# Kernel optimization log

Measured on AMD Instinct MI355X. Metric: run time of the kernel, lower is better.

The kernel has to match this reference:

```python
import jax, jax.numpy as jnp
import numpy as np

C_IN = 256
C_OUT = 256
NUM_HEADS = 4
C_HEAD = C_OUT // NUM_HEADS  # 64
ALPHA = 0.2
NEG_FILL = -9e15


def setup_inputs() -> dict:
    key = jax.random.key(0)
    k1, k2, k3, k4, k5 = jax.random.split(key, 5)
    B, N = 1, 4096
    node_feats = jax.random.normal(k1, (B, N, C_IN), dtype=jnp.float32)
    adj_matrix = jax.random.randint(k2, (B, N, N), 0, 2, dtype=jnp.int32)
    # xavier_uniform with gain=1.414 on projection weight (fan_in=C_IN, fan_out=C_OUT)
    lim_w = 1.414 * np.sqrt(6.0 / (C_IN + C_OUT))
    W = jax.random.uniform(k3, (C_IN, C_OUT), dtype=jnp.float32, minval=-lim_w, maxval=lim_w)
    b = jnp.zeros((C_OUT,), dtype=jnp.float32)
    lim_a = 1.414 * np.sqrt(6.0 / (NUM_HEADS + 2 * C_HEAD))
    a = jax.random.uniform(k4, (NUM_HEADS, 2 * C_HEAD), dtype=jnp.float32, minval=-lim_a, maxval=lim_a)
    return {"node_feats": node_feats, "adj_matrix": adj_matrix, "W": W, "b": b, "a": a}


def reference(node_feats, adj_matrix, W, b, a):
    B, N, _ = node_feats.shape
    # linear projection -> (B, N, H, C_HEAD)
    feats = (node_feats @ W + b).reshape(B, N, NUM_HEADS, C_HEAD)
    # attention logit for edge (i -> j): a_src . h_i + a_dst . h_j, per head
    a_src, a_dst = a[:, :C_HEAD], a[:, C_HEAD:]
    src = jnp.einsum('bnhc,hc->bnh', feats, a_src)  # indexed by row i
    dst = jnp.einsum('bnhc,hc->bnh', feats, a_dst)  # indexed by col j
    logits = src[:, :, None, :] + dst[:, None, :, :]  # (B, N, N, H)
    logits = jnp.where(logits >= 0, logits, ALPHA * logits)  # LeakyReLU(0.2)
    attn = jnp.where(adj_matrix[..., None] == 1, logits, NEG_FILL)
    probs = jax.nn.softmax(attn, axis=2)  # softmax over source nodes j
    out = jnp.einsum('bijh,bjhc->bihc', probs, feats)
    return out.reshape(B, N, NUM_HEADS * C_HEAD)  # concat heads
```

## Files before the change

kernel.cpp:

```cpp
#include <hip/hip_runtime.h>

#define NN 4096
#define C 256
#define NH 4
#define CH 64
#define JSPLIT 16
#define JSLICE (NN / JSPLIT)
#define NJT (JSLICE / 32)

typedef float f32x4 __attribute__((ext_vector_type(4)));
typedef __bf16 b16x8 __attribute__((ext_vector_type(8)));
typedef unsigned short u16x8 __attribute__((ext_vector_type(8)));
typedef unsigned int u32x4 __attribute__((ext_vector_type(4)));
typedef _Float16 f16x2 __attribute__((ext_vector_type(2)));

__device__ inline float fast_exp2(float x) {
#if __has_builtin(__builtin_amdgcn_exp2f)
  return __builtin_amdgcn_exp2f(x);
#else
  return exp2f(x);
#endif
}

__device__ inline unsigned pack2bf(float f0, float f1) {
  unsigned u0 = __float_as_uint(f0) + 0x8000u;
  unsigned u1 = __float_as_uint(f1) + 0x8000u;
  return __builtin_amdgcn_perm(u1, u0, 0x07060302u);
}

__global__ __launch_bounds__(256) void k_prep(
    const float* __restrict__ X, const float* __restrict__ W,
    unsigned short* __restrict__ Xbf, unsigned short* __restrict__ WT) {
  const int b = blockIdx.x, t = threadIdx.x;
  if (b < 1024) {
    const int idx = b * 256 + t;
    const float4 v = ((const float4*)X)[idx];
    uint2 st;
    st.x = pack2bf(v.x, v.y);
    st.y = pack2bf(v.z, v.w);
    ((uint2*)Xbf)[idx] = st;
  } else {
    const int c = b - 1024;
    const float w = W[(size_t)t * C + c];
    WT[(size_t)c * C + t] = (unsigned short)((__float_as_uint(w) + 0x8000u) >> 16);
  }
}

__global__ __launch_bounds__(256) void k_feats(
    const unsigned short* __restrict__ Xbf, const unsigned short* __restrict__ WT,
    const float* __restrict__ bias, const float* __restrict__ av,
    const int* __restrict__ adj, unsigned char* __restrict__ packed,
    unsigned short* __restrict__ F, float2* __restrict__ srcAB,
    float2* __restrict__ EdT2) {
  if (blockIdx.x >= 256) {
    const int idx = (blockIdx.x - 256) * 256 + threadIdx.x;
    const int4 a0 = *(const int4*)(adj + (size_t)idx * 8);
    const int4 a1 = *(const int4*)(adj + (size_t)idx * 8 + 4);
    unsigned m = 0;
    m |= (a0.x != 0) ? 1u : 0u;   m |= (a0.y != 0) ? 2u : 0u;
    m |= (a0.z != 0) ? 4u : 0u;   m |= (a0.w != 0) ? 8u : 0u;
    m |= (a1.x != 0) ? 16u : 0u;  m |= (a1.y != 0) ? 32u : 0u;
    m |= (a1.z != 0) ? 64u : 0u;  m |= (a1.w != 0) ? 128u : 0u;
    packed[idx] = (unsigned char)m;
    return;
  }
  const int i0 = blockIdx.x * 16;
  const int h = threadIdx.x >> 6;
  const int lane = threadIdx.x & 63;
  const int q = lane >> 4, n = lane & 15;
  const int c0 = h * CH;
  const float LOG2E = 1.4426950408889634f;

  const f32x4 zero = {0.f, 0.f, 0.f, 0.f};
  f32x4 acc[4];
#pragma unroll
  for (int g = 0; g < 4; ++g) acc[g] = zero;

  const unsigned short* ap = Xbf + (size_t)(i0 + n) * C + q * 8;
#pragma unroll
  for (int kt = 0; kt < 8; ++kt) {
    const b16x8 aF = __builtin_bit_cast(b16x8, *(const u16x8*)(ap + kt * 32));
#pragma unroll
    for (int g = 0; g < 4; ++g) {
      const b16x8 bF = __builtin_bit_cast(b16x8,
          *(const u16x8*)(WT + (size_t)(c0 + g * 16 + n) * C + kt * 32 + q * 8));
      acc[g] = __builtin_amdgcn_mfma_f32_16x16x32_bf16(aF, bF, acc[g], 0, 0, 0);
    }
  }

  float fb[4][4], asv[4], adv[4];
#pragma unroll
  for (int g = 0; g < 4; ++g) {
    const float bs = bias[c0 + g * 16 + n];
    asv[g] = av[h * 128 + g * 16 + n];
    adv[g] = av[h * 128 + 64 + g * 16 + n];
#pragma unroll
    for (int r = 0; r < 4; ++r) fb[g][r] = acc[g][r] + bs;
  }
  const int jt = i0 >> 5, half = (i0 >> 4) & 1;
  const int qp = half * 2 + (q >> 1);
#pragma unroll
  for (int g = 0; g < 4; ++g) {
    uint2 st;
    st.x = pack2bf(fb[g][0], fb[g][1]);
    st.y = pack2bf(fb[g][2], fb[g][3]);
    *(uint2*)(F + ((size_t)((jt * NH + h) * 4 + g)) * 512 + (qp * 16 + n) * 8 + 4 * (q & 1)) = st;
  }
#pragma unroll
  for (int r = 0; r < 4; ++r) {
    float p = 0.f, d = 0.f;
#pragma unroll
    for (int g = 0; g < 4; ++g) {
      p = fmaf(fb[g][r], asv[g], p);
      d = fmaf(fb[g][r], adv[g], d);
    }
#pragma unroll
    for (int m = 1; m < 16; m <<= 1) {
      p += __shfl_xor(p, m);
      d += __shfl_xor(d, m);
    }
    if (n == 0) {
      const int row = i0 + q * 4 + r;
      const float dL = d * LOG2E;
      EdT2[(size_t)h * NN + row] = make_float2(fast_exp2(dL), fast_exp2(0.2f * dL));
      const float x = p + 16.0f;
      const float m2 = fmaxf(x, 0.2f * x) * LOG2E;
      srcAB[(size_t)row * NH + h] = make_float2(
          fast_exp2(fmaf(p, LOG2E, -m2)),
          fast_exp2(fmaf(0.2f * p, LOG2E, -m2)));
    }
  }
}

__global__ __launch_bounds__(256, 4) void k_attn(
    const unsigned char* __restrict__ packed,
    const unsigned short* __restrict__ F,
    const float2* __restrict__ srcAB, const float2* __restrict__ EdT2,
    _Float16* __restrict__ pacc, float* __restrict__ lpart) {
  const int wgid = blockIdx.x;
  const int slice = (wgid & 7) + (((wgid >> 10) & 1) << 3);
  const int i0 = ((wgid >> 3) & 127) * 32;
  const int h = threadIdx.x >> 6;
  const int lane = threadIdx.x & 63;
  const int q = lane >> 4, n = lane & 15;
  const int jbase = slice * JSLICE;

  const int r0 = i0 + n, r1 = i0 + 16 + n;
  const float2 ab0 = srcAB[(size_t)r0 * NH + h];
  const float2 ab1 = srcAB[(size_t)r1 * NH + h];

  const f32x4 zero = {0.f, 0.f, 0.f, 0.f};
  f32x4 acc0[4], acc1[4], lacc0 = zero, lacc1 = zero;
#pragma unroll
  for (int g = 0; g < 4; ++g) { acc0[g] = zero; acc1[g] = zero; }

  u16x8 ou;
#pragma unroll
  for (int jj = 0; jj < 8; ++jj) ou[jj] = 0x3F80;
  const b16x8 ones = __builtin_bit_cast(b16x8, ou);

  const uint2 m20 = *(const uint2*)(packed + (size_t)r0 * 512 + (jbase >> 3) + q * 8);
  const uint2 m21 = *(const uint2*)(packed + (size_t)r1 * 512 + (jbase >> 3) + q * 8);

  const float* dp2 = (const float*)(EdT2 + (size_t)h * NN + jbase);
  const unsigned short* fp = F + ((size_t)((jbase >> 5) * NH + h) * 4) * 512 + lane * 8;

#pragma unroll
  for (int a = 0; a < 4; ++a) {
#pragma unroll
    for (int b = 0; b < 2; ++b) {
      const int jt = a * 2 + b;
      b16x8 bF[4];
#pragma unroll
      for (int g = 0; g < 4; ++g)
        bF[g] = __builtin_bit_cast(b16x8,
            *(const u16x8*)(fp + (size_t)(jt * NH * 4 + g) * 512));

      const int w0 = b ? (int)m20.y : (int)m20.x;
      const int w1 = b ? (int)m21.y : (int)m21.x;
      const unsigned Mb0 = (unsigned(__shfl(w0, a * 16 + n)) >> (q * 8)) & 0xffu;
      const unsigned Mb1 = (unsigned(__shfl(w1, a * 16 + n)) >> (q * 8)) & 0xffu;

      const float* dq = dp2 + jt * 64 + q * 16;
      const float4 dd0 = *(const float4*)(dq);
      const float4 dd1 = *(const float4*)(dq + 4);
      const float4 dd2 = *(const float4*)(dq + 8);
      const float4 dd3 = *(const float4*)(dq + 12);
      const float4 dd[4] = {dd0, dd1, dd2, dd3};

      u32x4 pk0, pk1;
#pragma unroll
      for (int k = 0; k < 4; ++k) {
        const float4 d = dd[k];
        const float e00 = (Mb0 & (1u << (2 * k))) ? fmaxf(d.x * ab0.x, d.y * ab0.y) : 0.f;
        const float e01 = (Mb0 & (2u << (2 * k))) ? fmaxf(d.z * ab0.x, d.w * ab0.y) : 0.f;
        const float e10 = (Mb1 & (1u << (2 * k))) ? fmaxf(d.x * ab1.x, d.y * ab1.y) : 0.f;
        const float e11 = (Mb1 & (2u << (2 * k))) ? fmaxf(d.z * ab1.x, d.w * ab1.y) : 0.f;
        pk0[k] = pack2bf(e00, e01);
        pk1[k] = pack2bf(e10, e11);
      }
      const b16x8 E0 = __builtin_bit_cast(b16x8, pk0);
      const b16x8 E1 = __builtin_bit_cast(b16x8, pk1);
#pragma unroll
      for (int g = 0; g < 4; ++g) {
        acc0[g] = __builtin_amdgcn_mfma_f32_16x16x32_bf16(E0, bF[g], acc0[g], 0, 0, 0);
        acc1[g] = __builtin_amdgcn_mfma_f32_16x16x32_bf16(E1, bF[g], acc1[g], 0, 0, 0);
      }
      lacc0 = __builtin_amdgcn_mfma_f32_16x16x32_bf16(E0, ones, lacc0, 0, 0, 0);
      lacc1 = __builtin_amdgcn_mfma_f32_16x16x32_bf16(E1, ones, lacc1, 0, 0, 0);
    }
  }

#pragma unroll
  for (int g = 0; g < 4; ++g)
#pragma unroll
    for (int r = 0; r < 4; ++r) {
      const int col = h * CH + g * 16 + n;
      pacc[((size_t)slice * NN + i0 + q * 4 + r) * C + col] = (_Float16)acc0[g][r];
      pacc[((size_t)slice * NN + i0 + 16 + q * 4 + r) * C + col] = (_Float16)acc1[g][r];
    }
  if (n == 0) {
#pragma unroll
    for (int r = 0; r < 4; ++r) {
      lpart[((size_t)slice * NN + i0 + q * 4 + r) * NH + h] = lacc0[r];
      lpart[((size_t)slice * NN + i0 + 16 + q * 4 + r) * NH + h] = lacc1[r];
    }
  }
}

__global__ __launch_bounds__(256) void k_final(
    const _Float16* __restrict__ pacc, const float* __restrict__ lpart,
    float* __restrict__ out) {
  const int t = threadIdx.x;
  const int row = blockIdx.x * 2 + (t >> 7);
  const int tc = t & 127;
  const int c2 = tc * 2;
  const int h = tc >> 5;
  float l = 0.f, sa0 = 0.f, sa1 = 0.f;
#pragma unroll
  for (int sp = 0; sp < JSPLIT; ++sp) {
    l += lpart[((size_t)sp * NN + row) * NH + h];
    const f16x2 v = *(const f16x2*)(pacc + ((size_t)sp * NN + row) * C + c2);
    sa0 += (float)v[0];
    sa1 += (float)v[1];
  }
  const float rl = 1.0f / l;
  *(float2*)(out + (size_t)row * C + c2) = make_float2(sa0 * rl, sa1 * rl);
}

extern "C" void kernel_launch(void* const* d_in, const int* in_sizes, int n_in,
                              void* d_out, int out_size, void* d_ws, size_t ws_size,
                              hipStream_t stream) {
  const float* nf   = (const float*)d_in[0];
  const int* adj    = (const int*)d_in[1];
  const float* W    = (const float*)d_in[2];
  const float* bias = (const float*)d_in[3];
  const float* av   = (const float*)d_in[4];
  float* out = (float*)d_out;

  char* ws = (char*)d_ws;
  unsigned char* packed  = (unsigned char*)ws;
  unsigned short* Xbf    = (unsigned short*)(ws + (2u << 20));
  unsigned short* WT     = (unsigned short*)(ws + (4u << 20));
  unsigned short* F      = (unsigned short*)(ws + (4u << 20) + (256u << 10));
  float2* srcAB = (float2*)(ws + (6u << 20) + (256u << 10));
  float2* EdT2  = (float2*)(ws + (6u << 20) + (384u << 10));
  float* lpart  = (float*)(ws + (6u << 20) + (512u << 10));
  _Float16* pacc = (_Float16*)(ws + (8u << 20));

  k_prep<<<1280, 256, 0, stream>>>(nf, W, Xbf, WT);
  k_feats<<<8448, 256, 0, stream>>>(Xbf, WT, bias, av, adj, packed, F, srcAB, EdT2);
  k_attn<<<2048, 256, 0, stream>>>(packed, F, srcAB, EdT2, pacc, lpart);
  k_final<<<NN / 2, 256, 0, stream>>>(pacc, lpart, out);
}
```

Measured before the change: 146.2 us.

## Share feature tiles across two row groups via double-buffered LDS staging

The attention kernel now uses 512-thread workgroups covering 64 rows, so two row groups share each feature tile. The tile is staged into LDS with direct global-to-LDS loads, double-buffered so the next tile loads while the current one feeds the MFMAs. This halves global reads of F per row and aims to overlap memory latency with compute. In exchange it adds a barrier every j-tile and 32KB of LDS per block, which may limit occupancy.

```diff
diff --git a/kernel.cpp b/kernel.cpp
--- a/kernel.cpp
+++ b/kernel.cpp
@@ -26,6 +26,12 @@
   unsigned u0 = __float_as_uint(f0) + 0x8000u;
   unsigned u1 = __float_as_uint(f1) + 0x8000u;
   return __builtin_amdgcn_perm(u1, u0, 0x07060302u);
+}
+
+__device__ inline void stage1k(const unsigned short* g, unsigned short* l) {
+  __builtin_amdgcn_global_load_lds(
+      (const __attribute__((address_space(1))) void*)g,
+      (__attribute__((address_space(3))) void*)l, 16, 0, 0);
 }
 
 __global__ __launch_bounds__(256) void k_prep(
@@ -132,20 +138,26 @@
   }
 }
 
-__global__ __launch_bounds__(256, 4) void k_attn(
+__global__ __launch_bounds__(512, 4) void k_attn(
     const unsigned char* __restrict__ packed,
     const unsigned short* __restrict__ F,
     const float2* __restrict__ srcAB, const float2* __restrict__ EdT2,
     _Float16* __restrict__ pacc, float* __restrict__ lpart) {
+  __shared__ unsigned short smem[2][16 * 512];
+
   const int wgid = blockIdx.x;
-  const int slice = (wgid & 7) + (((wgid >> 10) & 1) << 3);
-  const int i0 = ((wgid >> 3) & 127) * 32;
-  const int h = threadIdx.x >> 6;
-  const int lane = threadIdx.x & 63;
+  const int slice = (wgid & 7) | (((wgid >> 9) & 1) << 3);
+  const int i0 = ((wgid >> 3) & 63) * 64;
+  const int tid = threadIdx.x;
+  const int wv = tid >> 6;
+  const int h = wv & 3;
+  const int rg = wv >> 2;
+  const int lane = tid & 63;
   const int q = lane >> 4, n = lane & 15;
   const int jbase = slice * JSLICE;
-
-  const int r0 = i0 + n, r1 = i0 + 16 + n;
+  const int ib = i0 + rg * 32;
+
+  const int r0 = ib + n, r1 = ib + 16 + n;
   const float2 ab0 = srcAB[(size_t)r0 * NH + h];
   const float2 ab1 = srcAB[(size_t)r1 * NH + h];
 
@@ -163,52 +175,60 @@
   const uint2 m21 = *(const uint2*)(packed + (size_t)r1 * 512 + (jbase >> 3) + q * 8);
 
   const float* dp2 = (const float*)(EdT2 + (size_t)h * NN + jbase);
-  const unsigned short* fp = F + ((size_t)((jbase >> 5) * NH + h) * 4) * 512 + lane * 8;
-
-#pragma unroll
-  for (int a = 0; a < 4; ++a) {
-#pragma unroll
-    for (int b = 0; b < 2; ++b) {
-      const int jt = a * 2 + b;
-      b16x8 bF[4];
-#pragma unroll
-      for (int g = 0; g < 4; ++g)
-        bF[g] = __builtin_bit_cast(b16x8,
-            *(const u16x8*)(fp + (size_t)(jt * NH * 4 + g) * 512));
-
-      const int w0 = b ? (int)m20.y : (int)m20.x;
-      const int w1 = b ? (int)m21.y : (int)m21.x;
-      const unsigned Mb0 = (unsigned(__shfl(w0, a * 16 + n)) >> (q * 8)) & 0xffu;
-      const unsigned Mb1 = (unsigned(__shfl(w1, a * 16 + n)) >> (q * 8)) & 0xffu;
-
-      const float* dq = dp2 + jt * 64 + q * 16;
-      const float4 dd0 = *(const float4*)(dq);
-      const float4 dd1 = *(const float4*)(dq + 4);
-      const float4 dd2 = *(const float4*)(dq + 8);
-      const float4 dd3 = *(const float4*)(dq + 12);
-      const float4 dd[4] = {dd0, dd1, dd2, dd3};
-
-      u32x4 pk0, pk1;
-#pragma unroll
-      for (int k = 0; k < 4; ++k) {
-        const float4 d = dd[k];
-        const float e00 = (Mb0 & (1u << (2 * k))) ? fmaxf(d.x * ab0.x, d.y * ab0.y) : 0.f;
-        const float e01 = (Mb0 & (2u << (2 * k))) ? fmaxf(d.z * ab0.x, d.w * ab0.y) : 0.f;
-        const float e10 = (Mb1 & (1u << (2 * k))) ? fmaxf(d.x * ab1.x, d.y * ab1.y) : 0.f;
-        const float e11 = (Mb1 & (2u << (2 * k))) ? fmaxf(d.z * ab1.x, d.w * ab1.y) : 0.f;
-        pk0[k] = pack2bf(e00, e01);
-        pk1[k] = pack2bf(e10, e11);
-      }
-      const b16x8 E0 = __builtin_bit_cast(b16x8, pk0);
-      const b16x8 E1 = __builtin_bit_cast(b16x8, pk1);
-#pragma unroll
-      for (int g = 0; g < 4; ++g) {
-        acc0[g] = __builtin_amdgcn_mfma_f32_16x16x32_bf16(E0, bF[g], acc0[g], 0, 0, 0);
-        acc1[g] = __builtin_amdgcn_mfma_f32_16x16x32_bf16(E1, bF[g], acc1[g], 0, 0, 0);
-      }
-      lacc0 = __builtin_amdgcn_mfma_f32_16x16x32_bf16(E0, ones, lacc0, 0, 0, 0);
-      lacc1 = __builtin_amdgcn_mfma_f32_16x16x32_bf16(E1, ones, lacc1, 0, 0, 0);
-    }
+  const unsigned short* fpb = F + (size_t)(jbase >> 5) * (16 * 512);
+  const int ch0 = wv * 2, ch1 = wv * 2 + 1;
+
+  stage1k(fpb + (size_t)(0 * 16 + ch0) * 512 + lane * 8, &smem[0][ch0 * 512]);
+  stage1k(fpb + (size_t)(0 * 16 + ch1) * 512 + lane * 8, &smem[0][ch1 * 512]);
+
+#pragma unroll
+  for (int jt = 0; jt < NJT; ++jt) {
+    const int cur = jt & 1;
+    __syncthreads();
+    if (jt + 1 < NJT) {
+      stage1k(fpb + (size_t)((jt + 1) * 16 + ch0) * 512 + lane * 8, &smem[cur ^ 1][ch0 * 512]);
+      stage1k(fpb + (size_t)((jt + 1) * 16 + ch1) * 512 + lane * 8, &smem[cur ^ 1][ch1 * 512]);
+    }
+
+    b16x8 bF[4];
+#pragma unroll
+    for (int g = 0; g < 4; ++g)
+      bF[g] = __builtin_bit_cast(b16x8,
+          *(const u16x8*)(&smem[cur][(h * 4 + g) * 512 + lane * 8]));
+
+    const int a = jt >> 1, b = jt & 1;
+    const int w0 = b ? (int)m20.y : (int)m20.x;
+    const int w1 = b ? (int)m21.y : (int)m21.x;
+    const unsigned Mb0 = (unsigned(__shfl(w0, a * 16 + n)) >> (q * 8)) & 0xffu;
+    const unsigned Mb1 = (unsigned(__shfl(w1, a * 16 + n)) >> (q * 8)) & 0xffu;
+
+    const float* dq = dp2 + jt * 64 + q * 16;
+    const float4 dd0 = *(const float4*)(dq);
+    const float4 dd1 = *(const float4*)(dq + 4);
+    const float4 dd2 = *(const float4*)(dq + 8);
+    const float4 dd3 = *(const float4*)(dq + 12);
+    const float4 dd[4] = {dd0, dd1, dd2, dd3};
+
+    u32x4 pk0, pk1;
+#pragma unroll
+    for (int k = 0; k < 4; ++k) {
+      const float4 d = dd[k];
+      const float e00 = (Mb0 & (1u << (2 * k))) ? fmaxf(d.x * ab0.x, d.y * ab0.y) : 0.f;
+      const float e01 = (Mb0 & (2u << (2 * k))) ? fmaxf(d.z * ab0.x, d.w * ab0.y) : 0.f;
+      const float e10 = (Mb1 & (1u << (2 * k))) ? fmaxf(d.x * ab1.x, d.y * ab1.y) : 0.f;
+      const float e11 = (Mb1 & (2u << (2 * k))) ? fmaxf(d.z * ab1.x, d.w * ab1.y) : 0.f;
+      pk0[k] = pack2bf(e00, e01);
+      pk1[k] = pack2bf(e10, e11);
+    }
+    const b16x8 E0 = __builtin_bit_cast(b16x8, pk0);
+    const b16x8 E1 = __builtin_bit_cast(b16x8, pk1);
+#pragma unroll
+    for (int g = 0; g < 4; ++g) {
+      acc0[g] = __builtin_amdgcn_mfma_f32_16x16x32_bf16(E0, bF[g], acc0[g], 0, 0, 0);
+      acc1[g] = __builtin_amdgcn_mfma_f32_16x16x32_bf16(E1, bF[g], acc1[g], 0, 0, 0);
+    }
+    lacc0 = __builtin_amdgcn_mfma_f32_16x16x32_bf16(E0, ones, lacc0, 0, 0, 0);
+    lacc1 = __builtin_amdgcn_mfma_f32_16x16x32_bf16(E1, ones, lacc1, 0, 0, 0);
   }
 
 #pragma unroll
@@ -216,14 +236,14 @@
 #pragma unroll
     for (int r = 0; r < 4; ++r) {
       const int col = h * CH + g * 16 + n;
-      pacc[((size_t)slice * NN + i0 + q * 4 + r) * C + col] = (_Float16)acc0[g][r];
-      pacc[((size_t)slice * NN + i0 + 16 + q * 4 + r) * C + col] = (_Float16)acc1[g][r];
+      pacc[((size_t)slice * NN + ib + q * 4 + r) * C + col] = (_Float16)acc0[g][r];
+      pacc[((size_t)slice * NN + ib + 16 + q * 4 + r) * C + col] = (_Float16)acc1[g][r];
     }
   if (n == 0) {
 #pragma unroll
     for (int r = 0; r < 4; ++r) {
-      lpart[((size_t)slice * NN + i0 + q * 4 + r) * NH + h] = lacc0[r];
-      lpart[((size_t)slice * NN + i0 + 16 + q * 4 + r) * NH + h] = lacc1[r];
+      lpart[((size_t)slice * NN + ib + q * 4 + r) * NH + h] = lacc0[r];
+      lpart[((size_t)slice * NN + ib + 16 + q * 4 + r) * NH + h] = lacc1[r];
     }
   }
 }
@@ -270,6 +290,6 @@
 
   k_prep<<<1280, 256, 0, stream>>>(nf, W, Xbf, WT);
   k_feats<<<8448, 256, 0, stream>>>(Xbf, WT, bias, av, adj, packed, F, srcAB, EdT2);
-  k_attn<<<2048, 256, 0, stream>>>(packed, F, srcAB, EdT2, pacc, lpart);
+  k_attn<<<1024, 512, 0, stream>>>(packed, F, srcAB, EdT2, pacc, lpart);
   k_final<<<NN / 2, 256, 0, stream>>>(pacc, lpart, out);
 }
```

Result: no change. 147.8 us (+1.1%).
